# Kernel tuning notes

Measured on AMD Instinct MI355X. Metric: run time of the kernel, lower is better.

## Reference

```python
import jax, jax.numpy as jnp
import numpy as np
import math

B, S, HID = 4, 512, 768
H, D = 12, 64          # heads, head_size
I = 3072               # intermediate_size
EPS = 1e-12


def setup_inputs() -> dict:
    key = jax.random.key(0)
    ks = jax.random.split(key, 16)
    std = 0.02
    inp = {
        'hidden_states': jax.random.normal(ks[0], (B, S, HID), jnp.float32),
        'attention_mask': jnp.zeros((B, 1, 1, S), jnp.float32),
        'Wq': jax.random.normal(ks[1], (HID, HID), jnp.float32) * std,
        'bq': jnp.zeros((HID,), jnp.float32),
        'Wk': jax.random.normal(ks[2], (HID, HID), jnp.float32) * std,
        'bk': jnp.zeros((HID,), jnp.float32),
        'Wv': jax.random.normal(ks[3], (HID, HID), jnp.float32) * std,
        'bv': jnp.zeros((HID,), jnp.float32),
        'Wo': jax.random.normal(ks[4], (H, D, HID), jnp.float32) * std,  # per-head w_o
        'bo': jnp.zeros((H, HID), jnp.float32),
        'w_kp': jax.nn.softmax(jax.random.normal(ks[5], (H,), jnp.float32)),
        'w_a': jax.nn.softmax(jax.random.normal(ks[6], (H,), jnp.float32)),
        'Wi': jax.random.normal(ks[7], (HID, I), jnp.float32) * std,
        'bi': jnp.zeros((I,), jnp.float32),
        'Wout': jax.random.normal(ks[8], (I, HID), jnp.float32) * std,
        'bout': jnp.zeros((HID,), jnp.float32),
        'gamma': jnp.ones((HID,), jnp.float32),
        'beta': jnp.zeros((HID,), jnp.float32),
    }
    return inp


def _layernorm(x, gamma, beta):
    u = x.mean(-1, keepdims=True)
    s = jnp.mean((x - u) ** 2, axis=-1, keepdims=True)
    return gamma * (x - u) / jnp.sqrt(s + EPS) + beta


def _gelu(x):
    return x * 0.5 * (1.0 + jax.lax.erf(x / math.sqrt(2.0)))


def reference(hidden_states, attention_mask, Wq, bq, Wk, bk, Wv, bv,
              Wo, bo, w_kp, w_a, Wi, bi, Wout, bout, gamma, beta):
    # self-attention (eval mode: no dropout, no head_mask)
    q = (hidden_states @ Wq + bq).reshape(B, S, H, D)
    k = (hidden_states @ Wk + bk).reshape(B, S, H, D)
    v = (hidden_states @ Wv + bv).reshape(B, S, H, D)
    scores = jnp.einsum('bqhd,bkhd->bhqk', q, k) / math.sqrt(D)
    scores = scores + attention_mask  # additive mask, broadcast [B,1,1,S]
    probs = jax.nn.softmax(scores, axis=-1)
    ctx = jnp.einsum('bhqk,bkhd->bqhd', probs, v)  # [B,S,H,D]

    # per-head output projection w_o[i]: 64 -> 768, scaled by kappa
    head_out = jnp.einsum('bqhd,hdm->bqhm', ctx, Wo) + bo  # [B,S,H,HID]
    x = w_kp[None, None, :, None] * head_out
    # shared intermediate (gelu) + output linear, applied per head stream
    inter = _gelu(jnp.einsum('bqhm,mi->bqhi', x, Wi) + bi)  # [B,S,H,I]
    out = jnp.einsum('bqhi,im->bqhm', inter, Wout) + bout   # [B,S,H,HID]
    out = (w_a[None, None, :, None] * out).sum(axis=2)      # sum over heads

    return _layernorm(hidden_states + out, gamma, beta)
```

## Files before the change

kernel.cpp:

```cpp
#include <hip/hip_runtime.h>
#include <hip/hip_bf16.h>
#include <math.h>

typedef __hip_bfloat16 bf16;
typedef __attribute__((ext_vector_type(4))) float f32x4;
typedef __attribute__((ext_vector_type(8))) short short8;

#define HIDN 768
#define NTOK 2048
#define NH 12
#define HD 64
#define ISZ 3072
#define SEQ 512

__device__ __forceinline__ bf16 f2bf(float x){ return __float2bfloat16(x); }
__device__ __forceinline__ float gelu_fast(float x){
    float u = x * fmaf(x*x, -0.1029432f, -2.302208f);
    float e = exp2f(u);
    return x * __builtin_amdgcn_rcpf(1.0f + e);
}

__device__ __forceinline__ void gload16(const bf16* g, bf16* l){
    __builtin_amdgcn_global_load_lds(
        (const __attribute__((address_space(1))) unsigned int*)g,
        (__attribute__((address_space(3))) unsigned int*)l,
        16, 0, 0);
}

#define FENCE asm volatile("" ::: "memory")

template<int EPI>
__global__ __launch_bounds__(512)
void gemm_pipe(const bf16* __restrict__ A, const bf16* __restrict__ B,
               void* __restrict__ Cbase, const float* __restrict__ bias,
               int lda, int ldb, int ldc,
               long sAz, long sBz, long sCz)
{
    __shared__ __align__(16) char hlds[2*24576];
    int z = blockIdx.z;
    A += (long)z*sAz; B += (long)z*sBz;

    int nwg  = gridDim.x * gridDim.y;
    int orig = blockIdx.y * gridDim.x + blockIdx.x;
    int q8 = nwg >> 3, r8 = nwg & 7;
    int xcd = orig & 7, idx = orig >> 3;
    int wg = (xcd < r8 ? xcd*(q8+1) : r8*(q8+1) + (xcd-r8)*q8) + idx;
    int bn = wg % gridDim.x, bm = wg / gridDim.x;

    int t = threadIdx.x;
    int wave = t >> 6, lane = t & 63;
    int wm = (wave >> 1) << 5;
    int wn = (wave & 1) << 5;
    int lr = lane & 15, lg = lane >> 4;
    int x7 = lr & 7;
    int gb0 = ((lg    ) ^ x7) << 4;
    int gb1 = ((4 | lg) ^ x7) << 4;

    int srow = t >> 3;
    int glog = (t & 7) ^ (srow & 7);
    const bf16* Ag0 = A + (long)(bm*128 + srow)*lda + glog*8;
    const bf16* Ag1 = Ag0 + (long)64*lda;
    const bf16* Bg0 = B + (long)(bn*64 + srow)*ldb + glog*8;

#define PSTAGE(buf,kt) { \
    gload16(Ag0 + (kt)*64, (bf16*)(hlds + (buf)*24576 + t*16)); \
    gload16(Ag1 + (kt)*64, (bf16*)(hlds + (buf)*24576 + 8192 + t*16)); \
    gload16(Bg0 + (kt)*64, (bf16*)(hlds + (buf)*24576 + 16384 + t*16)); }

    PSTAGE(0, 0);

    f32x4 acc[2][2] = {};

    #pragma unroll
    for (int kt = 0; kt < 12; ++kt){
        if (kt < 11) PSTAGE((kt+1)&1, kt+1);
        if (kt < 11) asm volatile("s_waitcnt vmcnt(3)" ::: "memory");
        else         asm volatile("s_waitcnt vmcnt(0)" ::: "memory");
        FENCE; __builtin_amdgcn_s_barrier(); FENCE;

        const char* Lb = hlds + (kt&1)*24576;
        short8 af[2][2], bfr[2][2];
        #pragma unroll
        for (int m=0;m<2;m++){
            const char* pr = Lb + (wm + m*16 + lr)*128;
            af[m][0] = *(const short8*)(pr + gb0);
            af[m][1] = *(const short8*)(pr + gb1);
        }
        #pragma unroll
        for (int n=0;n<2;n++){
            const char* pr = Lb + 16384 + (wn + n*16 + lr)*128;
            bfr[n][0] = *(const short8*)(pr + gb0);
            bfr[n][1] = *(const short8*)(pr + gb1);
        }
        __builtin_amdgcn_s_setprio(1);
        #pragma unroll
        for (int m=0;m<2;m++)
            #pragma unroll
            for (int n=0;n<2;n++)
                #pragma unroll
                for (int kk=0;kk<2;kk++)
                    acc[m][n] = __builtin_amdgcn_mfma_f32_16x16x32_bf16(af[m][kk], bfr[n][kk], acc[m][n], 0,0,0);
        __builtin_amdgcn_s_setprio(0);
        FENCE; __builtin_amdgcn_s_barrier(); FENCE;
    }
#undef PSTAGE

    #pragma unroll
    for (int m=0;m<2;m++){
        #pragma unroll
        for (int n=0;n<2;n++){
            int col = bn*64 + wn + n*16 + lr;
            #pragma unroll
            for (int i=0;i<4;i++){
                long row = (long)bm*128 + wm + m*16 + lg*4 + i;
                ((float*)Cbase + (long)z*sCz)[row*ldc+col] = acc[m][n][i];
            }
        }
    }
}

__global__ __launch_bounds__(512)
void gemm_pre(const bf16* __restrict__ WiT, const bf16* __restrict__ Wobf,
              const bf16* __restrict__ bo_pad, const bf16* __restrict__ hbf,
              const bf16* __restrict__ WqkvT,
              bf16* __restrict__ WcT, float* __restrict__ bhc,
              bf16* __restrict__ qkv,
              const float* __restrict__ w_kp, const float* __restrict__ bi,
              const float* __restrict__ bqkv)
{
    __shared__ __align__(16) char hlds[2*24576];
    int bid = blockIdx.x;
    int mode, local, gx, nwg, ldc;
    const bf16 *A, *B;
    if (bid < 48){        mode=0; local=bid;     gx=48; nwg=48;  A=bo_pad; B=WiT;   ldc=ISZ; }
    else if (bid < 336){  mode=1; local=bid-48;  gx=12; nwg=288; A=WiT;    B=Wobf;  ldc=HIDN; }
    else {                mode=2; local=bid-336; gx=36; nwg=576; A=hbf;    B=WqkvT; ldc=3*HIDN; }

    int cpx = nwg >> 3;
    int wg = (local & 7)*cpx + (local >> 3);
    int bn = wg % gx, bm = wg / gx;

    int t = threadIdx.x;
    int wave = t >> 6, lane = t & 63;
    int wm = (wave >> 1) << 5;
    int wn = (wave & 1) << 5;
    int lr = lane & 15, lg = lane >> 4;
    int x7 = lr & 7;
    int gb0 = ((lg    ) ^ x7) << 4;
    int gb1 = ((4 | lg) ^ x7) << 4;

    int srow = t >> 3;
    int glog = (t & 7) ^ (srow & 7);
    const bf16* Ag0 = A + (long)(bm*128 + srow)*HIDN + glog*8;
    const bf16* Ag1 = Ag0 + (long)64*HIDN;
    const bf16* Bg0 = B + (long)(bn*64 + srow)*HIDN + glog*8;

#define PSTAGE(buf,kt) { \
    gload16(Ag0 + (kt)*64, (bf16*)(hlds + (buf)*24576 + t*16)); \
    gload16(Ag1 + (kt)*64, (bf16*)(hlds + (buf)*24576 + 8192 + t*16)); \
    gload16(Bg0 + (kt)*64, (bf16*)(hlds + (buf)*24576 + 16384 + t*16)); }

    PSTAGE(0, 0);

    f32x4 acc[2][2] = {};

    #pragma unroll
    for (int kt = 0; kt < 12; ++kt){
        if (kt < 11) PSTAGE((kt+1)&1, kt+1);
        if (kt < 11) asm volatile("s_waitcnt vmcnt(3)" ::: "memory");
        else         asm volatile("s_waitcnt vmcnt(0)" ::: "memory");
        FENCE; __builtin_amdgcn_s_barrier(); FENCE;

        const char* Lb = hlds + (kt&1)*24576;
        short8 af[2][2], bfr[2][2];
        #pragma unroll
        for (int m=0;m<2;m++){
            const char* pr = Lb + (wm + m*16 + lr)*128;
            af[m][0] = *(const short8*)(pr + gb0);
            af[m][1] = *(const short8*)(pr + gb1);
        }
        #pragma unroll
        for (int n=0;n<2;n++){
            const char* pr = Lb + 16384 + (wn + n*16 + lr)*128;
            bfr[n][0] = *(const short8*)(pr + gb0);
            bfr[n][1] = *(const short8*)(pr + gb1);
        }
        __builtin_amdgcn_s_setprio(1);
        #pragma unroll
        for (int m=0;m<2;m++)
            #pragma unroll
            for (int n=0;n<2;n++)
                #pragma unroll
                for (int kk=0;kk<2;kk++)
                    acc[m][n] = __builtin_amdgcn_mfma_f32_16x16x32_bf16(af[m][kk], bfr[n][kk], acc[m][n], 0,0,0);
        __builtin_amdgcn_s_setprio(0);
        FENCE; __builtin_amdgcn_s_barrier(); FENCE;
    }
#undef PSTAGE

    #pragma unroll
    for (int m=0;m<2;m++){
        #pragma unroll
        for (int n=0;n<2;n++){
            int col = bn*64 + wn + n*16 + lr;
            #pragma unroll
            for (int i=0;i<4;i++){
                long row = (long)bm*128 + wm + m*16 + lg*4 + i;
                float v = acc[m][n][i];
                if (mode == 0){
                    if (row < NH) bhc[row*ISZ+col] = fmaf(w_kp[row], v, bi[col]);
                } else if (mode == 1){
                    WcT[row*HIDN+col] = f2bf(v * w_kp[col>>6]);
                } else {
                    qkv[row*(3*HIDN)+col] = f2bf(v + bqkv[col]);
                }
            }
        }
    }
}

__global__ __launch_bounds__(128)
void flash_attn(const bf16* __restrict__ qkv, const bf16* __restrict__ Vt,
                const float* __restrict__ mask, bf16* __restrict__ ctx2)
{
    __shared__ __align__(16) char p_lds[4096];
    int z = blockIdx.y;
    int b = z / NH, h = z - b*NH;
    int t = threadIdx.x;
    int wave = t >> 6, lane = t & 63;
    int q0 = blockIdx.x*32 + wave*16;
    int lr = lane & 15, lg = lane >> 4;
    int x7 = lr & 7;
    int gb0 = ((lg    ) ^ x7) << 4;
    int gb1 = ((4 | lg) ^ x7) << 4;

    const bf16* Qp = qkv + (long)(b*SEQ + q0 + lr)*(3*HIDN) + h*HD + lg*8;
    short8 aq0 = *(const short8*)(Qp);
    short8 aq1 = *(const short8*)(Qp + 32);

    const bf16* Kb = qkv + (long)b*SEQ*(3*HIDN) + HIDN + h*HD + lg*8;
    const bf16* Vb = Vt + (long)z*HD*SEQ;
    const float* mb = mask + b*SEQ;
    char* pw = p_lds + wave*2048;

    f32x4 o[4] = {};
    float lsum[4] = {0.f,0.f,0.f,0.f};

    for (int kt = 0; kt < 8; ++kt){
        int kbase = kt*64;
        short8 bk0[4], bk1[4];
        #pragma unroll
        for (int nf=0;nf<4;nf++){
            const bf16* kp = Kb + (long)(kbase + nf*16 + lr)*(3*HIDN);
            bk0[nf] = *(const short8*)(kp);
            bk1[nf] = *(const short8*)(kp + 32);
        }
        f32x4 s[4] = {};
        #pragma unroll
        for (int nf=0;nf<4;nf++){
            s[nf] = __builtin_amdgcn_mfma_f32_16x16x32_bf16(aq0, bk0[nf], s[nf], 0,0,0);
            s[nf] = __builtin_amdgcn_mfma_f32_16x16x32_bf16(aq1, bk1[nf], s[nf], 0,0,0);
        }
        short8 bv0[4], bv1[4];
        #pragma unroll
        for (int nf=0;nf<4;nf++){
            const bf16* vp = Vb + (long)(nf*16 + lr)*SEQ + kbase + lg*8;
            bv0[nf] = *(const short8*)(vp);
            bv1[nf] = *(const short8*)(vp + 32);
        }
        #pragma unroll
        for (int nf=0;nf<4;nf++){
            float mkl = mb[kbase + nf*16 + lr] * 1.442695041f;
            int gk = nf*2 + (lr>>3);
            #pragma unroll
            for (int i=0;i<4;i++){
                int q = lg*4 + i;
                float e = exp2f(fmaf(s[nf][i], 0.18033688f, mkl));
                lsum[i] += e;
                *(bf16*)(pw + q*128 + ((gk ^ (q&7))<<4) + (lr&7)*2) = f2bf(e);
            }
        }
        short8 ap0 = *(const short8*)(pw + lr*128 + gb0);
        short8 ap1 = *(const short8*)(pw + lr*128 + gb1);
        #pragma unroll
        for (int nf=0;nf<4;nf++){
            o[nf] = __builtin_amdgcn_mfma_f32_16x16x32_bf16(ap0, bv0[nf], o[nf], 0,0,0);
            o[nf] = __builtin_amdgcn_mfma_f32_16x16x32_bf16(ap1, bv1[nf], o[nf], 0,0,0);
        }
    }
    #pragma unroll
    for (int i=0;i<4;i++){
        float v = lsum[i];
        v += __shfl_xor(v, 1, 64);
        v += __shfl_xor(v, 2, 64);
        v += __shfl_xor(v, 4, 64);
        v += __shfl_xor(v, 8, 64);
        lsum[i] = __builtin_amdgcn_rcpf(v);
    }
    bf16* Cp = ctx2 + (long)(b*SEQ + q0)*HIDN + h*HD;
    #pragma unroll
    for (int nf=0;nf<4;nf++)
        #pragma unroll
        for (int i=0;i<4;i++)
            Cp[(long)(lg*4+i)*HIDN + nf*16 + lr] = f2bf(o[nf][i] * lsum[i]);
}

__global__ __launch_bounds__(512)
void gemm_heads(const bf16* __restrict__ A, const bf16* __restrict__ B,
                bf16* __restrict__ S, const float* __restrict__ bhc,
                const float* __restrict__ w_a)
{
    __shared__ __align__(16) char hlds[2*24576 + 3072];
    char* bhcl = hlds + 49152;

    int orig = blockIdx.y*48 + blockIdx.x;
    int xcd = orig & 7, idx = orig >> 3;
    int bm = ((xcd >> 2) << 3) + idx/12;
    int bn = (xcd & 3)*12 + idx%12;

    int t = threadIdx.x;
    int wave = t >> 6, lane = t & 63;
    int wm = (wave >> 1) << 5;
    int wn = (wave & 1) << 5;
    int lr = lane & 15, lg = lane >> 4;
    int x7 = lr & 7;
    int gb0 = ((lg    ) ^ x7) << 4;
    int gb1 = ((4 | lg) ^ x7) << 4;

    int srow = t >> 3;
    int glog = (t & 7) ^ (srow & 7);
    const bf16* Ag0 = A + (long)(bm*128 + srow)*HIDN + glog*8;
    const bf16* Ag1 = Ag0 + (long)64*HIDN;
    const bf16* Bg0 = B + (long)(bn*64 + srow)*HIDN + glog*8;

    float wav[NH];
    #pragma unroll
    for (int h=0;h<NH;h++) wav[h] = w_a[h];

    if (t < 192){
        const float* src = bhc + (t>>4)*ISZ + bn*64 + (t&15)*4;
        gload16((const bf16*)src, (bf16*)(bhcl + t*16));
    }

#define HSTAGE(buf,h) { \
    gload16(Ag0 + (h)*64, (bf16*)(hlds + (buf)*24576 + t*16)); \
    gload16(Ag1 + (h)*64, (bf16*)(hlds + (buf)*24576 + 8192 + t*16)); \
    gload16(Bg0 + (h)*64, (bf16*)(hlds + (buf)*24576 + 16384 + t*16)); }

    HSTAGE(0, 0);

    const f32x4 zz = {};
    f32x4 acc[2][2] = {};
    f32x4 sacc[2][2] = {};

    #pragma unroll
    for (int h = 0; h < NH; ++h){
        if (h < NH-1) HSTAGE((h+1)&1, h+1);
        if (h > 0){
            float bh0 = *(const float*)(bhcl + (h-1)*256 + (wn+lr)*4);
            float bh1 = *(const float*)(bhcl + (h-1)*256 + (wn+16+lr)*4);
            #pragma unroll
            for (int m=0;m<2;m++)
                #pragma unroll
                for (int n=0;n<2;n++)
                    #pragma unroll
                    for (int i=0;i<4;i++){
                        float v = acc[m][n][i] + (n ? bh1 : bh0);
                        sacc[m][n][i] = fmaf(wav[h-1], gelu_fast(v), sacc[m][n][i]);
                    }
        }
        if (h < NH-1) asm volatile("s_waitcnt vmcnt(3)" ::: "memory");
        else          asm volatile("s_waitcnt vmcnt(0)" ::: "memory");
        FENCE; __builtin_amdgcn_s_barrier(); FENCE;

        const char* Lb = hlds + (h&1)*24576;
        short8 af[2][2], bfr[2][2];
        #pragma unroll
        for (int m=0;m<2;m++){
            const char* pr = Lb + (wm + m*16 + lr)*128;
            af[m][0] = *(const short8*)(pr + gb0);
            af[m][1] = *(const short8*)(pr + gb1);
        }
        #pragma unroll
        for (int n=0;n<2;n++){
            const char* pr = Lb + 16384 + (wn + n*16 + lr)*128;
            bfr[n][0] = *(const short8*)(pr + gb0);
            bfr[n][1] = *(const short8*)(pr + gb1);
        }
        __builtin_amdgcn_s_setprio(1);
        #pragma unroll
        for (int m=0;m<2;m++)
            #pragma unroll
            for (int n=0;n<2;n++)
                acc[m][n] = __builtin_amdgcn_mfma_f32_16x16x32_bf16(af[m][1], bfr[n][1],
                    __builtin_amdgcn_mfma_f32_16x16x32_bf16(af[m][0], bfr[n][0], zz, 0,0,0), 0,0,0);
        __builtin_amdgcn_s_setprio(0);
        FENCE; __builtin_amdgcn_s_barrier(); FENCE;
    }
#undef HSTAGE

    {
        float bh0 = *(const float*)(bhcl + (NH-1)*256 + (wn+lr)*4);
        float bh1 = *(const float*)(bhcl + (NH-1)*256 + (wn+16+lr)*4);
        #pragma unroll
        for (int m=0;m<2;m++)
            #pragma unroll
            for (int n=0;n<2;n++)
                #pragma unroll
                for (int i=0;i<4;i++){
                    float v = acc[m][n][i] + (n ? bh1 : bh0);
                    sacc[m][n][i] = fmaf(wav[NH-1], gelu_fast(v), sacc[m][n][i]);
                }
    }

    #pragma unroll
    for (int m=0;m<2;m++)
        #pragma unroll
        for (int n=0;n<2;n++)
            #pragma unroll
            for (int i=0;i<4;i++){
                long row = (long)bm*128 + wm + m*16 + lg*4 + i;
                S[row*ISZ + bn*64 + wn + n*16 + lr] = f2bf(sacc[m][n][i]);
            }
}

#define NPREP (NTOK*HIDN + HIDN*HIDN + 128*HIDN + 3*HIDN)
__global__ __launch_bounds__(256)
void prep_all(const float* __restrict__ Wq, const float* __restrict__ Wk,
              const float* __restrict__ Wv, const float* __restrict__ Wi,
              const float* __restrict__ Wout,
              bf16* __restrict__ WqkvT, bf16* __restrict__ WiT,
              bf16* __restrict__ WoutT,
              const float* __restrict__ hidden, const float* __restrict__ Wo,
              const float* __restrict__ bq, const float* __restrict__ bk,
              const float* __restrict__ bv, const float* __restrict__ bo,
              bf16* __restrict__ hbf, bf16* __restrict__ Wobf,
              float* __restrict__ bqkv, bf16* __restrict__ bo_pad)
{
    __shared__ float tile[32][33];
    int bid = blockIdx.x;
    if (bid >= 6336){
        int i = (bid-6336)*256 + threadIdx.x;
        const int n1 = NTOK*HIDN, n2 = HIDN*HIDN, n3 = 128*HIDN;
        if (i < n1) hbf[i] = f2bf(hidden[i]);
        int j = i - n1;
        if (j >= 0 && j < n2) Wobf[j] = f2bf(Wo[j]);
        int k = i - n1 - n2;
        if (k >= 0 && k < n3) bo_pad[k] = (k < NH*HIDN) ? f2bf(bo[k]) : f2bf(0.f);
        int l = i - n1 - n2 - n3;
        if (l >= 0 && l < 3*HIDN)
            bqkv[l] = (l < HIDN) ? bq[l] : (l < 2*HIDN ? bk[l-HIDN] : bv[l-2*HIDN]);
        return;
    }
    const float* src; bf16* dst; int R, C, ct, rem;
    if (bid < 1728){
        int z = bid / 576; rem = bid - z*576;
        src = (z==0) ? Wq : ((z==1) ? Wk : Wv);
        dst = WqkvT + (long)z*HIDN*HIDN;
        R = HIDN; C = HIDN; ct = 24;
    } else if (bid < 4032){
        rem = bid - 1728; src = Wi; dst = WiT; R = HIDN; C = ISZ; ct = 96;
    } else {
        rem = bid - 4032; src = Wout; dst = WoutT; R = ISZ; C = HIDN; ct = 24;
    }
    int c0 = (rem % ct)*32, r0 = (rem / ct)*32;
    int tx = threadIdx.x & 31, ty = threadIdx.x >> 5;
    #pragma unroll
    for (int i=0;i<32;i+=8) tile[ty+i][tx] = src[(long)(r0+ty+i)*C + c0+tx];
    __syncthreads();
    #pragma unroll
    for (int i=0;i<32;i+=8) dst[(long)(c0+ty+i)*R + r0+tx] = f2bf(tile[tx][ty+i]);
}

__global__ __launch_bounds__(256)
void transpose_v(const bf16* __restrict__ qkv, bf16* __restrict__ Vt)
{
    __shared__ bf16 tile[32][33];
    int za = blockIdx.z; int b = za/NH, h = za - b*NH;
    const bf16* src = qkv + (long)b*SEQ*3*HIDN + 2*HIDN + h*HD;
    bf16* dst = Vt + (long)za*HD*SEQ;
    int d0 = blockIdx.x*32, s0 = blockIdx.y*32;
    int tx = threadIdx.x & 31, ty = threadIdx.x >> 5;
    #pragma unroll
    for (int i=0;i<32;i+=8) tile[ty+i][tx] = src[(long)(s0+ty+i)*(3*HIDN) + d0+tx];
    __syncthreads();
    #pragma unroll
    for (int i=0;i<32;i+=8) dst[(long)(d0+ty+i)*SEQ + s0+tx] = tile[tx][ty+i];
}

__global__ __launch_bounds__(256)
void add_ln(const float* __restrict__ hidden, const float* __restrict__ part,
            const float* __restrict__ bout, const float* __restrict__ w_a,
            const float* __restrict__ gamma, const float* __restrict__ beta,
            float* __restrict__ out)
{
    __shared__ float red[8];
    int row = blockIdx.x;
    int t = threadIdx.x;
    int wave = t>>6, lane = t&63;
    float swa = 0.f;
    #pragma unroll
    for (int h=0;h<NH;h++) swa += w_a[h];
    float x[3];
    float sum = 0.f;
    #pragma unroll
    for (int j=0;j<3;j++){
        int c = j*256 + t;
        long idx = (long)row*HIDN + c;
        float acc = part[idx] + part[idx + (long)NTOK*HIDN]
                  + part[idx + 2L*NTOK*HIDN] + part[idx + 3L*NTOK*HIDN];
        x[j] = hidden[idx] + acc + swa*bout[c];
        sum += x[j];
    }
    #pragma unroll
    for (int o=32;o>0;o>>=1) sum += __shfl_xor(sum,o,64);
    if (lane==0) red[wave]=sum;
    __syncthreads();
    sum = red[0]+red[1]+red[2]+red[3];
    float u = sum * (1.0f/768.0f);
    float vs = 0.f;
    #pragma unroll
    for (int j=0;j<3;j++){ float d = x[j]-u; vs += d*d; }
    #pragma unroll
    for (int o=32;o>0;o>>=1) vs += __shfl_xor(vs,o,64);
    __syncthreads();
    if (lane==0) red[4+wave]=vs;
    __syncthreads();
    vs = red[4]+red[5]+red[6]+red[7];
    float rstd = rsqrtf(vs*(1.0f/768.0f) + 1e-12f);
    #pragma unroll
    for (int j=0;j<3;j++){
        int c = j*256 + t;
        out[(long)row*HIDN + c] = gamma[c]*(x[j]-u)*rstd + beta[c];
    }
}

extern "C" void kernel_launch(void* const* d_in, const int* in_sizes, int n_in,
                              void* d_out, int out_size, void* d_ws, size_t ws_size,
                              hipStream_t stream)
{
    const float* hidden = (const float*)d_in[0];
    const float* mask   = (const float*)d_in[1];
    const float* Wq = (const float*)d_in[2];
    const float* bq = (const float*)d_in[3];
    const float* Wk = (const float*)d_in[4];
    const float* bk = (const float*)d_in[5];
    const float* Wv = (const float*)d_in[6];
    const float* bv = (const float*)d_in[7];
    const float* Wo = (const float*)d_in[8];
    const float* bo = (const float*)d_in[9];
    const float* w_kp = (const float*)d_in[10];
    const float* w_a  = (const float*)d_in[11];
    const float* Wi = (const float*)d_in[12];
    const float* bi = (const float*)d_in[13];
    const float* Wout = (const float*)d_in[14];
    const float* boutp = (const float*)d_in[15];
    const float* gamma = (const float*)d_in[16];
    const float* beta  = (const float*)d_in[17];
    float* out = (float*)d_out;

    char* w = (char*)d_ws;
    auto alloc = [&](size_t bytes)->char* {
        char* p = w; w += (bytes + 255) & ~(size_t)255; return p;
    };
    bf16*  hbf    = (bf16*) alloc((size_t)NTOK*HIDN*2);
    bf16*  WqkvT  = (bf16*) alloc((size_t)3*HIDN*HIDN*2);
    float* bqkv   = (float*)alloc((size_t)3*HIDN*4);
    bf16*  WiT    = (bf16*) alloc((size_t)ISZ*HIDN*2);
    bf16*  WoutT  = (bf16*) alloc((size_t)HIDN*ISZ*2);
    bf16*  Wobf   = (bf16*) alloc((size_t)HIDN*HIDN*2);
    bf16*  WcT    = (bf16*) alloc((size_t)ISZ*HIDN*2);
    bf16*  bo_pad = (bf16*) alloc((size_t)128*HIDN*2);
    float* bhc    = (float*)alloc((size_t)NH*ISZ*4);
    float* part   = (float*)alloc((size_t)4*NTOK*HIDN*4);
    bf16*  qkv    = (bf16*) alloc((size_t)NTOK*3*HIDN*2);
    bf16*  ctx2   = (bf16*) alloc((size_t)NTOK*HIDN*2);
    bf16*  Sbuf   = (bf16*) alloc((size_t)NTOK*ISZ*2);
    bf16*  Vt     = (bf16*) alloc((size_t)NH*4*HD*SEQ*2);

    prep_all<<<6336 + (NPREP+255)/256, 256, 0, stream>>>(
        Wq, Wk, Wv, Wi, Wout, WqkvT, WiT, WoutT,
        hidden, Wo, bq, bk, bv, bo, hbf, Wobf, bqkv, bo_pad);

    gemm_pre<<<912, 512, 0, stream>>>(
        WiT, Wobf, bo_pad, hbf, WqkvT,
        WcT, bhc, qkv, w_kp, bi, bqkv);

    transpose_v<<<dim3(2,16,48), 256, 0, stream>>>(qkv, Vt);
    flash_attn<<<dim3(SEQ/32, 48), 128, 0, stream>>>(qkv, Vt, mask, ctx2);

    gemm_heads<<<dim3(ISZ/64, NTOK/128), 512, 0, stream>>>(
        ctx2, WcT, Sbuf, bhc, w_a);

    gemm_pipe<1><<<dim3(HIDN/64, NTOK/128, 4), 512, 0, stream>>>(
        Sbuf, WoutT, part, nullptr,
        ISZ, ISZ, HIDN,
        768, 768, (long)NTOK*HIDN);

    add_ln<<<NTOK, 256, 0, stream>>>(hidden, part, boutp, w_a, gamma, beta, out);
}
```

Measured before the change: 132.5 us.

## Vectorize add_ln with float4, remap gemm_heads XCD swizzle, chain MFMA accumulators

The add_ln kernel now runs 192 threads per row, each loading and storing float4 values. This cuts the instruction count and drops one barrier. In gemm_heads, the hard-coded XCD/tile swizzle is replaced by a generic mapping that gives each XCD a contiguous chunk of the workgroup range. The MFMA chain now accumulates into acc, which is zeroed after the GELU epilogue, instead of starting from a zero vector. These are several small, unrelated tweaks: the swizzle change may shift L2 locality, and the add_ln and MFMA changes mainly reduce instruction overhead.

```diff
diff --git a/kernel.cpp b/kernel.cpp
--- a/kernel.cpp
+++ b/kernel.cpp
@@ -313,10 +313,11 @@
     __shared__ __align__(16) char hlds[2*24576 + 3072];
     char* bhcl = hlds + 49152;
 
-    int orig = blockIdx.y*48 + blockIdx.x;
-    int xcd = orig & 7, idx = orig >> 3;
-    int bm = ((xcd >> 2) << 3) + idx/12;
-    int bn = (xcd & 3)*12 + idx%12;
+    int nwg  = gridDim.x * gridDim.y;
+    int orig = blockIdx.y * gridDim.x + blockIdx.x;
+    int cpx = nwg >> 3;
+    int wg = (orig & 7)*cpx + (orig >> 3);
+    int bn = wg % gridDim.x, bm = wg / gridDim.x;
 
     int t = threadIdx.x;
     int wave = t >> 6, lane = t & 63;
@@ -349,7 +350,6 @@
 
     HSTAGE(0, 0);
 
-    const f32x4 zz = {};
     f32x4 acc[2][2] = {};
     f32x4 sacc[2][2] = {};
 
@@ -367,6 +367,7 @@
                     for (int i=0;i<4;i++){
                         float v = acc[m][n][i] + (n ? bh1 : bh0);
                         sacc[m][n][i] = fmaf(wav[h-1], gelu_fast(v), sacc[m][n][i]);
+                        acc[m][n][i] = 0.f;
                     }
         }
         if (h < NH-1) asm volatile("s_waitcnt vmcnt(3)" ::: "memory");
@@ -392,8 +393,9 @@
         for (int m=0;m<2;m++)
             #pragma unroll
             for (int n=0;n<2;n++)
-                acc[m][n] = __builtin_amdgcn_mfma_f32_16x16x32_bf16(af[m][1], bfr[n][1],
-                    __builtin_amdgcn_mfma_f32_16x16x32_bf16(af[m][0], bfr[n][0], zz, 0,0,0), 0,0,0);
+                #pragma unroll
+                for (int kk=0;kk<2;kk++)
+                    acc[m][n] = __builtin_amdgcn_mfma_f32_16x16x32_bf16(af[m][kk], bfr[n][kk], acc[m][n], 0,0,0);
         __builtin_amdgcn_s_setprio(0);
         FENCE; __builtin_amdgcn_s_barrier(); FENCE;
     }
@@ -488,51 +490,54 @@
     for (int i=0;i<32;i+=8) dst[(long)(d0+ty+i)*SEQ + s0+tx] = tile[tx][ty+i];
 }
 
-__global__ __launch_bounds__(256)
-void add_ln(const float* __restrict__ hidden, const float* __restrict__ part,
-            const float* __restrict__ bout, const float* __restrict__ w_a,
-            const float* __restrict__ gamma, const float* __restrict__ beta,
-            float* __restrict__ out)
-{
-    __shared__ float red[8];
+__global__ __launch_bounds__(192)
+void add_ln(const float4* __restrict__ hidden, const float4* __restrict__ part,
+            const float4* __restrict__ bout, const float* __restrict__ w_a,
+            const float4* __restrict__ gamma, const float4* __restrict__ beta,
+            float4* __restrict__ out)
+{
+    __shared__ float red[6];
     int row = blockIdx.x;
     int t = threadIdx.x;
-    int wave = t>>6, lane = t&63;
+    int wave = t >> 6, lane = t & 63;
     float swa = 0.f;
     #pragma unroll
     for (int h=0;h<NH;h++) swa += w_a[h];
-    float x[3];
-    float sum = 0.f;
-    #pragma unroll
-    for (int j=0;j<3;j++){
-        int c = j*256 + t;
-        long idx = (long)row*HIDN + c;
-        float acc = part[idx] + part[idx + (long)NTOK*HIDN]
-                  + part[idx + 2L*NTOK*HIDN] + part[idx + 3L*NTOK*HIDN];
-        x[j] = hidden[idx] + acc + swa*bout[c];
-        sum += x[j];
-    }
+
+    long idx = (long)row*192 + t;
+    float4 x = hidden[idx];
+    #pragma unroll
+    for (int z=0;z<4;z++){
+        float4 p = part[(long)z*NTOK*192 + idx];
+        x.x += p.x; x.y += p.y; x.z += p.z; x.w += p.w;
+    }
+    float4 bo4 = bout[t];
+    x.x += swa*bo4.x; x.y += swa*bo4.y; x.z += swa*bo4.z; x.w += swa*bo4.w;
+
+    float sum = x.x + x.y + x.z + x.w;
     #pragma unroll
     for (int o=32;o>0;o>>=1) sum += __shfl_xor(sum,o,64);
-    if (lane==0) red[wave]=sum;
+    if (lane==0) red[wave] = sum;
     __syncthreads();
-    sum = red[0]+red[1]+red[2]+red[3];
+    sum = red[0] + red[1] + red[2];
     float u = sum * (1.0f/768.0f);
-    float vs = 0.f;
-    #pragma unroll
-    for (int j=0;j<3;j++){ float d = x[j]-u; vs += d*d; }
+
+    float dx = x.x-u, dy = x.y-u, dz = x.z-u, dw = x.w-u;
+    float vs = dx*dx + dy*dy + dz*dz + dw*dw;
     #pragma unroll
     for (int o=32;o>0;o>>=1) vs += __shfl_xor(vs,o,64);
+    if (lane==0) red[3+wave] = vs;
     __syncthreads();
-    if (lane==0) red[4+wave]=vs;
-    __syncthreads();
-    vs = red[4]+red[5]+red[6]+red[7];
+    vs = red[3] + red[4] + red[5];
     float rstd = rsqrtf(vs*(1.0f/768.0f) + 1e-12f);
-    #pragma unroll
-    for (int j=0;j<3;j++){
-        int c = j*256 + t;
-        out[(long)row*HIDN + c] = gamma[c]*(x[j]-u)*rstd + beta[c];
-    }
+
+    float4 g = gamma[t], b = beta[t];
+    float4 r;
+    r.x = g.x*dx*rstd + b.x;
+    r.y = g.y*dy*rstd + b.y;
+    r.z = g.z*dz*rstd + b.z;
+    r.w = g.w*dw*rstd + b.w;
+    out[idx] = r;
 }
 
 extern "C" void kernel_launch(void* const* d_in, const int* in_sizes, int n_in,
@@ -597,5 +602,7 @@
         ISZ, ISZ, HIDN,
         768, 768, (long)NTOK*HIDN);
 
-    add_ln<<<NTOK, 256, 0, stream>>>(hidden, part, boutp, w_a, gamma, beta, out);
-}
+    add_ln<<<NTOK, 192, 0, stream>>>(
+        (const float4*)hidden, (const float4*)part, (const float4*)boutp,
+        w_a, (const float4*)gamma, (const float4*)beta, (float4*)out);
+}
```

New measurement: 133.8 us. About the same (+0.9%).
